# Kernel tuning notes

Measured on AMD Instinct MI355X. Metric: run time of the kernel, lower is better.

## Reference

```python
import jax, jax.numpy as jnp
import numpy as np

NUM_ITERATIONS = 4
STEP = 1
N_NODES = 50000
N_EDGES = 800000
D_FEAT = 64


def setup_inputs() -> dict:
    key = jax.random.key(0)
    k1, k2, k3 = jax.random.split(key, 3)
    x = jax.random.normal(k1, (N_NODES, D_FEAT), dtype=jnp.float32)
    src = jax.random.randint(k2, (N_EDGES,), 0, N_NODES, dtype=jnp.int64)
    dst = jax.random.randint(k3, (N_EDGES,), 0, N_NODES, dtype=jnp.int64)
    edge_index = jnp.stack([src, dst], axis=0)
    return {"x": x, "edge_index": edge_index}


def _wl_conv(x, src, dst, n_nodes):
    # continuous WL: x_i' = 0.5 * (x_i + mean_{j in N(i)} x_j)
    msg = x[src]  # [E, D] gather of neighbor features
    summed = jax.ops.segment_sum(msg, dst, num_segments=n_nodes)  # [N, D]
    deg = jax.ops.segment_sum(jnp.ones_like(dst, dtype=x.dtype), dst,
                              num_segments=n_nodes)  # [N]
    mean = summed / jnp.maximum(deg, 1.0)[:, None]  # isolated nodes -> 0
    return 0.5 * (x + mean)


def reference(x, edge_index):
    n_nodes = x.shape[0]
    src, dst = edge_index[0], edge_index[1]
    feats = [x]
    for _ in range(NUM_ITERATIONS):
        for _ in range(STEP):
            x = _wl_conv(x, src, dst, n_nodes)
        feats.append(x)
    return jnp.concatenate(feats, axis=-1)  # [N, (num_iterations+1)*D]
```

## Files before the change

### kernel.cpp

```cpp
#include <hip/hip_runtime.h>

constexpr int N = 50000;
constexpr int E = 800000;
constexpr int D = 64;
constexpr int DOUT = 320;
constexpr int CAPD = 128;
constexpr int ITER_BLOCKS = 2048;
constexpr int SCAN_BLOCKS = (N + 255) / 256;

__device__ __forceinline__ unsigned short f2bf(float f) {
    unsigned int u = __float_as_uint(f);
    unsigned int r = (u + 0x7fffu + ((u >> 16) & 1u)) >> 16;
    return (unsigned short)r;
}
__device__ __forceinline__ unsigned int pack2(float a, float b) {
    return (unsigned int)f2bf(a) | ((unsigned int)f2bf(b) << 16);
}
__device__ __forceinline__ float bflo(unsigned int u) { return __uint_as_float(u << 16); }
__device__ __forceinline__ float bfhi(unsigned int u) { return __uint_as_float(u & 0xFFFF0000u); }

__global__ __launch_bounds__(256) void build_csr_kernel(const int* __restrict__ ei32,
                                                        int* __restrict__ cnt,
                                                        unsigned short* __restrict__ csr) {
    int lane = threadIdx.x & 63;
    int wv = ei32[2 * lane + 1];
    int is64 = (__ballot(wv != 0) == 0ULL) ? 1 : 0;
    int i = blockIdx.x * 256 + threadIdx.x;
    if (i < E) {
        int s = is64 ? ei32[2 * i] : ei32[i];
        int d = is64 ? ei32[2 * (E + i)] : ei32[E + i];
        int r = atomicAdd(&cnt[d], 1);
        if (r < CAPD) csr[(size_t)d * CAPD + r] = (unsigned short)s;
    }
}


__global__ __launch_bounds__(256) void convert_kernel(const float* __restrict__ x,
                                                      float* __restrict__ out,
                                                      unsigned int* __restrict__ mirror) {
    int i = blockIdx.x * 256 + threadIdx.x;
    if (i < N * 16) {
        int n = i >> 4, j = i & 15;
        float4 v = ((const float4*)x)[i];
        ((float4*)(out + (size_t)n * DOUT))[j] = v;
        uint2 m = make_uint2(pack2(v.x, v.y), pack2(v.z, v.w));
        ((uint2*)(mirror + (size_t)n * 32))[j] = m;
    }
}


__global__ __launch_bounds__(256) void wl_iter_bf16_kernel(
    const unsigned int* __restrict__ min_,
    unsigned int* __restrict__ mout,
    const float* __restrict__ self_in,
    float* __restrict__ xout,
    const int* __restrict__ cnt, const unsigned short* __restrict__ csr) {
    int gw = blockIdx.x * 4 + (threadIdx.x >> 6);
    int lane = threadIdx.x & 63;
    int g = lane >> 3;
    int fi = lane & 7;
    const int NW = ITER_BLOCKS * 4;

    int deg_cur = (gw < N) ? min(cnt[gw], CAPD) : 0;
    for (int w = gw; w < N; w += NW) {
        int wn = w + NW;
        int deg_nxt = (wn < N) ? min(cnt[wn], CAPD) : 0;
        int deg = deg_cur;
        size_t base = (size_t)w * CAPD;

        float a[8], b[8];
#pragma unroll
        for (int k = 0; k < 8; ++k) { a[k] = 0.f; b[k] = 0.f; }

#define ACC8(u, arr)                                                     \
        arr[0] += bflo(u.x); arr[1] += bfhi(u.x);                        \
        arr[2] += bflo(u.y); arr[3] += bfhi(u.y);                        \
        arr[4] += bflo(u.z); arr[5] += bfhi(u.z);                        \
        arr[6] += bflo(u.w); arr[7] += bfhi(u.w);

        int e = g;
        for (; e + 8 < deg; e += 16) {
            int s0 = csr[base + e], s1 = csr[base + e + 8];
            uint4 u0 = *(const uint4*)(min_ + (size_t)s0 * 32 + fi * 4);
            uint4 u1 = *(const uint4*)(min_ + (size_t)s1 * 32 + fi * 4);
            ACC8(u0, a); ACC8(u1, b);
        }
        if (e < deg) {
            int s = csr[base + e];
            uint4 u = *(const uint4*)(min_ + (size_t)s * 32 + fi * 4);
            ACC8(u, a);
        }
#undef ACC8
#pragma unroll
        for (int k = 0; k < 8; ++k) {
            a[k] += b[k];
            a[k] += __shfl_xor(a[k], 8);
            a[k] += __shfl_xor(a[k], 16);
            a[k] += __shfl_xor(a[k], 32);
        }
        float inv = (deg > 0) ? 0.5f / (float)deg : 0.0f;
        if (g == 0) {
            const float* srow = self_in + (size_t)w * DOUT + fi * 8;
            float4 s0 = *(const float4*)(srow);
            float4 s1 = *(const float4*)(srow + 4);
            float r0 = 0.5f * s0.x + inv * a[0];
            float r1 = 0.5f * s0.y + inv * a[1];
            float r2 = 0.5f * s0.z + inv * a[2];
            float r3 = 0.5f * s0.w + inv * a[3];
            float r4 = 0.5f * s1.x + inv * a[4];
            float r5 = 0.5f * s1.y + inv * a[5];
            float r6 = 0.5f * s1.z + inv * a[6];
            float r7 = 0.5f * s1.w + inv * a[7];
            float* drow = xout + (size_t)w * DOUT + fi * 8;
            *(float4*)(drow)     = make_float4(r0, r1, r2, r3);
            *(float4*)(drow + 4) = make_float4(r4, r5, r6, r7);
            if (mout) {
                uint4 m = make_uint4(pack2(r0, r1), pack2(r2, r3),
                                     pack2(r4, r5), pack2(r6, r7));
                *(uint4*)(mout + (size_t)w * 32 + fi * 4) = m;
            }
        }
        deg_cur = deg_nxt;
    }
}


__global__ void detect_kernel(const int* __restrict__ ei32, int* __restrict__ flag) {
    if (blockIdx.x == 0 && threadIdx.x == 0) {
        int s = 0;
        for (int k = 0; k < 128; ++k) s |= ei32[2 * k + 1];
        *flag = (s == 0) ? 1 : 0;
    }
}
__device__ __forceinline__ int load_src(const int* ei32, int is64, int i) {
    return is64 ? ei32[2 * i] : ei32[i];
}
__device__ __forceinline__ int load_dst(const int* ei32, int is64, int i) {
    return is64 ? ei32[2 * (E + i)] : ei32[E + i];
}

__global__ __launch_bounds__(256) void hist_kernel(const int* __restrict__ ei32,
                                                   const int* __restrict__ flag,
                                                   int* __restrict__ cnt) {
    int i = blockIdx.x * 256 + threadIdx.x;
    int is64 = *flag;
    if (i < E) atomicAdd(&cnt[load_dst(ei32, is64, i)], 1);
}

__global__ __launch_bounds__(256) void scan1_kernel(const int* __restrict__ cnt,
                                                    int* __restrict__ offs,
                                                    int* __restrict__ P) {
    __shared__ int sm[256];
    int t = threadIdx.x;
    int i = blockIdx.x * 256 + t;
    int v = (i < N) ? cnt[i] : 0;
    sm[t] = v; __syncthreads();
    for (int o = 1; o < 256; o <<= 1) {
        int u = (t >= o) ? sm[t - o] : 0;
        __syncthreads();
        sm[t] += u;
        __syncthreads();
    }
    if (i < N) offs[i] = sm[t] - v;
    if (t == 255) P[blockIdx.x] = sm[255];
}

__global__ __launch_bounds__(256) void scan2_kernel(int* __restrict__ P,
                                                    int* __restrict__ offs) {
    __shared__ int sm[256];
    int t = threadIdx.x;
    int v = (t < SCAN_BLOCKS) ? P[t] : 0;
    sm[t] = v; __syncthreads();
    for (int o = 1; o < 256; o <<= 1) {
        int u = (t >= o) ? sm[t - o] : 0;
        __syncthreads();
        sm[t] += u;
        __syncthreads();
    }
    if (t < SCAN_BLOCKS) P[t] = sm[t] - v;
    if (t == 255) offs[N] = sm[255];
}

__global__ __launch_bounds__(256) void scan3_kernel(int* __restrict__ offs,
                                                    const int* __restrict__ P) {
    int i = blockIdx.x * 256 + threadIdx.x;
    if (i < N) offs[i] += P[blockIdx.x];
}

__global__ __launch_bounds__(256) void scatter_kernel(const int* __restrict__ ei32,
                                                      const int* __restrict__ flag,
                                                      const int* __restrict__ offs,
                                                      int* __restrict__ cursor,
                                                      int* __restrict__ csr) {
    int i = blockIdx.x * 256 + threadIdx.x;
    int is64 = *flag;
    if (i < E) {
        int d = load_dst(ei32, is64, i);
        int p = atomicAdd(&cursor[d], 1);
        csr[offs[d] + p] = load_src(ei32, is64, i);
    }
}

__global__ __launch_bounds__(256) void chunk0_kernel(const float* __restrict__ x,
                                                     float* __restrict__ out) {
    int i = blockIdx.x * 256 + threadIdx.x;
    if (i < N * 16) {
        int n = i >> 4, j = i & 15;
        float4 v = ((const float4*)x)[i];
        ((float4*)(out + (size_t)n * DOUT))[j] = v;
    }
}

__global__ __launch_bounds__(256) void wl_iter_kernel(
    const float* __restrict__ xin, float* __restrict__ xout,
    const int* __restrict__ offs, const int* __restrict__ csr) {
    int w = blockIdx.x * 4 + (threadIdx.x >> 6);
    if (w >= N) return;
    int lane = threadIdx.x & 63;
    int g = lane >> 4, fi = lane & 15;
    int beg = offs[w], end = offs[w + 1];
    float4 a0 = make_float4(0.f, 0.f, 0.f, 0.f);
    float4 a1 = make_float4(0.f, 0.f, 0.f, 0.f);
    int e = beg + g;
    for (; e + 4 < end; e += 8) {
        int s0 = csr[e], s1 = csr[e + 4];
        float4 v0 = *(const float4*)(xin + (size_t)s0 * DOUT + fi * 4);
        float4 v1 = *(const float4*)(xin + (size_t)s1 * DOUT + fi * 4);
        a0.x += v0.x; a0.y += v0.y; a0.z += v0.z; a0.w += v0.w;
        a1.x += v1.x; a1.y += v1.y; a1.z += v1.z; a1.w += v1.w;
    }
    if (e < end) {
        int s = csr[e];
        float4 v = *(const float4*)(xin + (size_t)s * DOUT + fi * 4);
        a0.x += v.x; a0.y += v.y; a0.z += v.z; a0.w += v.w;
    }
    float4 acc;
    acc.x = a0.x + a1.x; acc.y = a0.y + a1.y;
    acc.z = a0.z + a1.z; acc.w = a0.w + a1.w;
    acc.x += __shfl_xor(acc.x, 16); acc.y += __shfl_xor(acc.y, 16);
    acc.z += __shfl_xor(acc.z, 16); acc.w += __shfl_xor(acc.w, 16);
    acc.x += __shfl_xor(acc.x, 32); acc.y += __shfl_xor(acc.y, 32);
    acc.z += __shfl_xor(acc.z, 32); acc.w += __shfl_xor(acc.w, 32);
    int deg = end - beg;
    float inv = (deg > 0) ? 0.5f / (float)deg : 0.0f;
    if (g == 0) {
        float4 s4 = *(const float4*)(xin + (size_t)w * DOUT + fi * 4);
        float4 r;
        r.x = 0.5f * s4.x + inv * acc.x;
        r.y = 0.5f * s4.y + inv * acc.y;
        r.z = 0.5f * s4.z + inv * acc.z;
        r.w = 0.5f * s4.w + inv * acc.w;
        *(float4*)(xout + (size_t)w * DOUT + fi * 4) = r;
    }
}


extern "C" void kernel_launch(void* const* d_in, const int* in_sizes, int n_in,
                              void* d_out, int out_size, void* d_ws, size_t ws_size,
                              hipStream_t stream) {
    const float* x  = (const float*)d_in[0];
    const int* ei32 = (const int*)d_in[1];
    float* out = (float*)d_out;

    int* cnt = (int*)d_ws;
    unsigned short* csr = (unsigned short*)(cnt + N);
    unsigned int* mirA = (unsigned int*)((char*)csr + (size_t)N * CAPD * 2);
    unsigned int* mirB = mirA + (size_t)N * 32;
    size_t need = (size_t)N * 4 + (size_t)N * CAPD * 2 + (size_t)2 * N * 32 * 4;

    dim3 b256(256);
    dim3 gE((E + 255) / 256);
    dim3 gIter(ITER_BLOCKS);
    dim3 gConv((N * 16 + 255) / 256);

    if (ws_size >= need) {
        hipMemsetAsync(cnt, 0, (size_t)N * 4, stream);
        build_csr_kernel<<<gE, b256, 0, stream>>>(ei32, cnt, csr);
        convert_kernel<<<gConv, b256, 0, stream>>>(x, out, mirA);
        wl_iter_bf16_kernel<<<gIter, b256, 0, stream>>>(
            mirA, mirB, out + 0 * D, out + 1 * D, cnt, csr);
        wl_iter_bf16_kernel<<<gIter, b256, 0, stream>>>(
            mirB, mirA, out + 1 * D, out + 2 * D, cnt, csr);
        wl_iter_bf16_kernel<<<gIter, b256, 0, stream>>>(
            mirA, mirB, out + 2 * D, out + 3 * D, cnt, csr);
        wl_iter_bf16_kernel<<<gIter, b256, 0, stream>>>(
            mirB, (unsigned int*)nullptr, out + 3 * D, out + 4 * D, cnt, csr);
    } else {
        int* flag  = (int*)d_ws;
        int* fcnt  = flag + 16;
        int* foffs = fcnt + N;
        int* P     = foffs + (N + 1);
        int* fcsr  = P + 256;
        detect_kernel<<<1, 64, 0, stream>>>(ei32, flag);
        hipMemsetAsync(fcnt, 0, (size_t)N * 4, stream);
        hist_kernel<<<gE, b256, 0, stream>>>(ei32, flag, fcnt);
        scan1_kernel<<<dim3(SCAN_BLOCKS), b256, 0, stream>>>(fcnt, foffs, P);
        scan2_kernel<<<1, b256, 0, stream>>>(P, foffs);
        scan3_kernel<<<dim3(SCAN_BLOCKS), b256, 0, stream>>>(foffs, P);
        hipMemsetAsync(fcnt, 0, (size_t)N * 4, stream);
        scatter_kernel<<<gE, b256, 0, stream>>>(ei32, flag, foffs, fcnt, fcsr);
        chunk0_kernel<<<gConv, b256, 0, stream>>>(x, out);
        for (int c = 1; c <= 4; ++c) {
            wl_iter_kernel<<<dim3((N + 3) / 4), b256, 0, stream>>>(
                out + (size_t)(c - 1) * D, out + (size_t)c * D, foffs, fcsr);
        }
    }
}
```

Baseline: 231.2 us.

## Partition CSR build by XCC so each die handles its own destination range

```diff
diff --git a/kernel.cpp b/kernel.cpp
--- a/kernel.cpp
+++ b/kernel.cpp
@@ -5,6 +5,10 @@
 constexpr int D = 64;
 constexpr int DOUT = 320;
 constexpr int CAPD = 128;
+constexpr int NODES_PER_TEAM = 6250;
+constexpr int CHUNK = 512;
+constexpr int NCHUNK = (E + CHUNK - 1) / CHUNK;
+constexpr int BUILD_BLOCKS = 2048;
 constexpr int ITER_BLOCKS = 2048;
 constexpr int SCAN_BLOCKS = (N + 255) / 256;
 
@@ -19,18 +23,34 @@
 __device__ __forceinline__ float bflo(unsigned int u) { return __uint_as_float(u << 16); }
 __device__ __forceinline__ float bfhi(unsigned int u) { return __uint_as_float(u & 0xFFFF0000u); }
 
-__global__ __launch_bounds__(256) void build_csr_kernel(const int* __restrict__ ei32,
-                                                        int* __restrict__ cnt,
-                                                        unsigned short* __restrict__ csr) {
+__global__ __launch_bounds__(256) void build_csr_team_kernel(
+    const int* __restrict__ ei32,
+    int* __restrict__ tctr,
+    int* __restrict__ cnt,
+    unsigned short* __restrict__ csr) {
     int lane = threadIdx.x & 63;
     int wv = ei32[2 * lane + 1];
     int is64 = (__ballot(wv != 0) == 0ULL) ? 1 : 0;
-    int i = blockIdx.x * 256 + threadIdx.x;
-    if (i < E) {
-        int s = is64 ? ei32[2 * i] : ei32[i];
-        int d = is64 ? ei32[2 * (E + i)] : ei32[E + i];
-        int r = atomicAdd(&cnt[d], 1);
-        if (r < CAPD) csr[(size_t)d * CAPD + r] = (unsigned short)s;
+    int xcc;
+    asm("s_getreg_b32 %0, hwreg(HW_REG_XCC_ID)" : "=s"(xcc));
+    xcc &= 7;
+    __shared__ int sh;
+    for (;;) {
+        if (threadIdx.x == 0) sh = atomicAdd(&tctr[xcc * 16], 1);
+        __syncthreads();
+        int c = sh;
+        __syncthreads();
+        if (c >= NCHUNK) break;
+        int base = c * CHUNK;
+        int lim = min(base + CHUNK, E);
+        for (int i = base + (int)threadIdx.x; i < lim; i += 256) {
+            int s = is64 ? ei32[2 * i] : ei32[i];
+            int d = is64 ? ei32[2 * (E + i)] : ei32[E + i];
+            if (d / NODES_PER_TEAM == xcc) {
+                int r = atomicAdd(&cnt[d], 1);
+                if (r < CAPD) csr[(size_t)d * CAPD + r] = (unsigned short)s;
+            }
+        }
     }
 }
 
@@ -262,11 +282,13 @@
     const int* ei32 = (const int*)d_in[1];
     float* out = (float*)d_out;
 
-    int* cnt = (int*)d_ws;
+    int* tctr = (int*)d_ws;
+    int* cnt  = tctr + 128;
     unsigned short* csr = (unsigned short*)(cnt + N);
     unsigned int* mirA = (unsigned int*)((char*)csr + (size_t)N * CAPD * 2);
     unsigned int* mirB = mirA + (size_t)N * 32;
-    size_t need = (size_t)N * 4 + (size_t)N * CAPD * 2 + (size_t)2 * N * 32 * 4;
+    size_t need = (size_t)(128 + N) * 4 + (size_t)N * CAPD * 2 +
+                  (size_t)2 * N * 32 * 4;
 
     dim3 b256(256);
     dim3 gE((E + 255) / 256);
@@ -274,8 +296,9 @@
     dim3 gConv((N * 16 + 255) / 256);
 
     if (ws_size >= need) {
-        hipMemsetAsync(cnt, 0, (size_t)N * 4, stream);
-        build_csr_kernel<<<gE, b256, 0, stream>>>(ei32, cnt, csr);
+        hipMemsetAsync(tctr, 0, (size_t)(128 + N) * 4, stream);
+        build_csr_team_kernel<<<dim3(BUILD_BLOCKS), b256, 0, stream>>>(
+            ei32, tctr, cnt, csr);
         convert_kernel<<<gConv, b256, 0, stream>>>(x, out, mirA);
         wl_iter_bf16_kernel<<<gIter, b256, 0, stream>>>(
             mirA, mirB, out + 0 * D, out + 1 * D, cnt, csr);
```

Measured after the change: 251.6 us. +8.8%, slower.
